# Performance work log

Measured on AMD Instinct MI355X. Metric: run time of the kernel, lower is better.

The kernel has to match this reference:

```python
import jax, jax.numpy as jnp
import numpy as np

HIDDEN = 1024
NUM_HEADS = 16
HEAD_DIM = HIDDEN // NUM_HEADS
EPS = 1e-05


def setup_inputs() -> dict:
    key = jax.random.key(0)
    ks = jax.random.split(key, 6)
    B, S = 4, 2048
    x = jax.random.normal(ks[0], (B, S, HIDDEN), dtype=jnp.float32)
    # trunc_normal_(std=0.02) approximated by scaled normal
    w_in = jax.random.normal(ks[1], (3 * HIDDEN, HIDDEN), dtype=jnp.float32) * 0.02
    b_in = jax.random.normal(ks[2], (3 * HIDDEN,), dtype=jnp.float32) * 0.02
    w_norm = jnp.ones((HIDDEN,), dtype=jnp.float32)
    lim = 1.0 / np.sqrt(HIDDEN)
    w_out = jax.random.uniform(ks[3], (HIDDEN, HIDDEN), dtype=jnp.float32, minval=-lim, maxval=lim)
    b_out = jax.random.uniform(ks[4], (HIDDEN,), dtype=jnp.float32, minval=-lim, maxval=lim)
    return {"x": x, "w_in": w_in, "b_in": b_in, "w_norm": w_norm, "w_out": w_out, "b_out": b_out}


def _rms_norm(x, w, eps):
    var = jnp.mean(jnp.square(x), axis=-1, keepdims=True)
    return x * jax.lax.rsqrt(var + eps) * w


def reference(x, w_in, b_in, w_norm, w_out, b_out):
    B, S, _ = x.shape
    xn = _rms_norm(x, w_norm, EPS)
    qkv = jnp.einsum('bsd,ed->bse', xn, w_in) + b_in  # [B,S,3*HIDDEN]
    q, k, v = jnp.split(qkv, 3, axis=-1)
    # [B,S,H*D] -> [B,H,S,D]
    def split_heads(t):
        return t.reshape(B, S, NUM_HEADS, HEAD_DIM).transpose(0, 2, 1, 3)
    q, k, v = split_heads(q), split_heads(k), split_heads(v)
    scale = 1.0 / np.sqrt(HEAD_DIM)
    scores = jnp.einsum('bhqd,bhkd->bhqk', q, k) * scale
    attn = jax.nn.softmax(scores, axis=-1)
    o = jnp.einsum('bhqk,bhkd->bhqd', attn, v)
    o = o.transpose(0, 2, 1, 3).reshape(B, S, HIDDEN)
    return jnp.einsum('bsd,ed->bse', o, w_out) + b_out
```

## Files before the change

### kernel.cpp

```cpp
#include <hip/hip_runtime.h>
#include <stdint.h>

typedef short bf16x4 __attribute__((ext_vector_type(4)));
typedef short bf16x8 __attribute__((ext_vector_type(8)));
typedef _Float16 f16x8 __attribute__((ext_vector_type(8)));
typedef float f32x4 __attribute__((ext_vector_type(4)));
typedef float f32x16 __attribute__((ext_vector_type(16)));
typedef unsigned int u32x4 __attribute__((ext_vector_type(4)));
typedef unsigned int u32x2 __attribute__((ext_vector_type(2)));

#if __has_builtin(__builtin_amdgcn_exp2f)
#define EXP2 __builtin_amdgcn_exp2f
#else
#define EXP2 exp2f
#endif

__device__ __forceinline__ short f2bf(float f) {
  union { float f; uint32_t u; } v; v.f = f;
  uint32_t r = (v.u + 0x7fffu + ((v.u >> 16) & 1u)) >> 16;
  return (short)(uint16_t)r;
}

__device__ __forceinline__ unsigned cvtpk_bf16(float lo, float hi) {
  unsigned r;
  asm("v_cvt_pk_bf16_f32 %0, %1, %2" : "=v"(r) : "v"(lo), "v"(hi));
  return r;
}

#if __has_builtin(__builtin_amdgcn_permlane32_swap)
__device__ __forceinline__ void plane32_swap(unsigned& a, unsigned& b) {
  u32x2 r = __builtin_amdgcn_permlane32_swap(a, b, false, false);
  a = r[0]; b = r[1];
}
__device__ __forceinline__ float xhalf_max(float x) {
  unsigned xu = __builtin_bit_cast(unsigned, x);
  u32x2 r = __builtin_amdgcn_permlane32_swap(xu, xu, false, false);
  return fmaxf(__builtin_bit_cast(float, r[0]), __builtin_bit_cast(float, r[1]));
}
__device__ __forceinline__ float xhalf_sum(float x) {
  unsigned xu = __builtin_bit_cast(unsigned, x);
  u32x2 r = __builtin_amdgcn_permlane32_swap(xu, xu, false, false);
  return __builtin_bit_cast(float, r[0]) + __builtin_bit_cast(float, r[1]);
}
#else
__device__ __forceinline__ void plane32_swap(unsigned& a, unsigned& b) {
  asm("s_nop 1\n\tv_permlane32_swap_b32 %0, %1" : "+v"(a), "+v"(b));
}
__device__ __forceinline__ float xhalf_max(float x) { return fmaxf(x, __shfl_xor(x, 32, 64)); }
__device__ __forceinline__ float xhalf_sum(float x) { return x + __shfl_xor(x, 32, 64); }
#endif

__device__ __forceinline__ float fmax3(float a, float b, float c) {
  return fmaxf(fmaxf(a, b), c);
}

__device__ __forceinline__ f32x16 zero16() {
  f32x16 z;
#pragma unroll
  for (int i = 0; i < 16; ++i) z[i] = 0.f;
  return z;
}

__device__ __forceinline__ void gld_lds16(const void* g, void* l) {
  __builtin_amdgcn_global_load_lds(
      (__attribute__((address_space(1))) const void*)g,
      (__attribute__((address_space(3))) void*)l, 16, 0, 0);
}

__global__ __launch_bounds__(256) void k_rmsnorm(const float* __restrict__ x,
                                                 const float* __restrict__ wn,
                                                 short* __restrict__ xn) {
  const int row = blockIdx.x;
  const int t = threadIdx.x;
  const float4 v = reinterpret_cast<const float4*>(x + (size_t)row * 1024)[t];
  float ss = v.x * v.x + v.y * v.y + v.z * v.z + v.w * v.w;
#pragma unroll
  for (int m = 32; m >= 1; m >>= 1) ss += __shfl_xor(ss, m, 64);
  __shared__ float red[4];
  if ((t & 63) == 0) red[t >> 6] = ss;
  __syncthreads();
  const float tot = red[0] + red[1] + red[2] + red[3];
  const float rr = rsqrtf(tot * (1.0f / 1024.0f) + 1e-5f);
  const float4 g = reinterpret_cast<const float4*>(wn)[t];
  bf16x4 o;
  o[0] = f2bf(v.x * rr * g.x);
  o[1] = f2bf(v.y * rr * g.y);
  o[2] = f2bf(v.z * rr * g.z);
  o[3] = f2bf(v.w * rr * g.w);
  reinterpret_cast<bf16x4*>(xn + (size_t)row * 1024)[t] = o;
}

__global__ __launch_bounds__(256) void k_cast_bf(const float* __restrict__ in,
                                                 short* __restrict__ out, int n4) {
  int i = blockIdx.x * 256 + threadIdx.x;
  if (i >= n4) return;
  float4 v = reinterpret_cast<const float4*>(in)[i];
  bf16x4 o;
  o[0] = f2bf(v.x); o[1] = f2bf(v.y); o[2] = f2bf(v.z); o[3] = f2bf(v.w);
  reinterpret_cast<bf16x4*>(out)[i] = o;
}

__global__ __launch_bounds__(256) void k_cast_f16(const float* __restrict__ in,
                                                  _Float16* __restrict__ out, int n4) {
  int i = blockIdx.x * 256 + threadIdx.x;
  if (i >= n4) return;
  float4 v = reinterpret_cast<const float4*>(in)[i];
  _Float16 o[4] = {(_Float16)v.x, (_Float16)v.y, (_Float16)v.z, (_Float16)v.w};
  reinterpret_cast<ulong1*>(out)[i] = *reinterpret_cast<ulong1*>(o);
}

__global__ __launch_bounds__(256) void k_gemm_qkv(const short* __restrict__ A,
                                                  const short* __restrict__ B,
                                                  const float* __restrict__ bias,
                                                  short* __restrict__ qb,
                                                  short* __restrict__ kb,
                                                  short* __restrict__ vb) {
  __shared__ __align__(16) short As[128 * 32];
  __shared__ __align__(16) short Bs[128 * 32];
  const int t = threadIdx.x;
  const int orig = blockIdx.y * 24 + blockIdx.x;
  const int swz = (orig & 7) * 192 + (orig >> 3);
  const long bn0 = (long)(swz % 24) * 128;
  const long bm0 = (long)(swz / 24) * 128;
  const int w = t >> 6, l = t & 63;
  const int wr = (w >> 1) * 64, wc = (w & 1) * 64;
  const int lm = l & 15, h = l >> 4;
  f32x4 acc[4][4];
#pragma unroll
  for (int i = 0; i < 4; ++i)
#pragma unroll
    for (int j = 0; j < 4; ++j) acc[i][j] = (f32x4){0.f, 0.f, 0.f, 0.f};
  const int srow = t >> 2, scol = (t & 3) * 8;
  const short* Ag = A + (bm0 + srow) * 1024 + scol;
  const short* Bg = B + (bn0 + srow) * 1024 + scol;
  short* AsP = As + t * 8;
  short* BsP = Bs + t * 8;
  for (int kt = 0; kt < 32; ++kt) {
    const int k0 = kt << 5;
    gld_lds16(Ag + k0, AsP);
    gld_lds16(Ag + k0 + 64 * 1024, AsP + 2048);
    gld_lds16(Bg + k0, BsP);
    gld_lds16(Bg + k0 + 64 * 1024, BsP + 2048);
    __syncthreads();
    bf16x8 af[4], bfr[4];
#pragma unroll
    for (int mi = 0; mi < 4; ++mi)
      af[mi] = *reinterpret_cast<const bf16x8*>(As + (wr + mi * 16 + lm) * 32 + h * 8);
#pragma unroll
    for (int ni = 0; ni < 4; ++ni)
      bfr[ni] = *reinterpret_cast<const bf16x8*>(Bs + (wc + ni * 16 + lm) * 32 + h * 8);
    __builtin_amdgcn_s_setprio(1);
#pragma unroll
    for (int mi = 0; mi < 4; ++mi)
#pragma unroll
      for (int ni = 0; ni < 4; ++ni)
        acc[mi][ni] = __builtin_amdgcn_mfma_f32_16x16x32_bf16(af[mi], bfr[ni], acc[mi][ni], 0, 0, 0);
    __builtin_amdgcn_s_setprio(0);
    __syncthreads();
  }
#pragma unroll
  for (int ni = 0; ni < 4; ++ni) {
    const int ncol = (int)bn0 + wc + ni * 16 + lm;
    const float bv = bias[ncol];
    const int which = ncol >> 10;
    const int e = ncol & 1023;
#pragma unroll
    for (int mi = 0; mi < 4; ++mi) {
#pragma unroll
      for (int r = 0; r < 4; ++r) {
        const long mrow = bm0 + wr + mi * 16 + h * 4 + r;
        const float val = acc[mi][ni][r] + bv;
        const long off = (((mrow >> 11) * 16 + (e >> 6)) * 2048 + (mrow & 2047)) * 64 + (e & 63);
        if (which == 0) qb[off] = f2bf(val * 0.18033688011112042f);
        else if (which == 1) kb[off] = f2bf(val);
        else vb[off] = f2bf(val);
      }
    }
  }
}

__global__ __launch_bounds__(256) void k_gemm_out(const _Float16* __restrict__ A,
                                                  const _Float16* __restrict__ B,
                                                  const float* __restrict__ bias,
                                                  float* __restrict__ outp) {
  __shared__ __align__(16) _Float16 As[128 * 32];
  __shared__ __align__(16) _Float16 Bs[128 * 32];
  const int t = threadIdx.x;
  const int orig = blockIdx.y * 8 + blockIdx.x;
  const int swz = (orig & 7) * 64 + (orig >> 3);
  const long bn0 = (long)(swz % 8) * 128;
  const long bm0 = (long)(swz / 8) * 128;
  const int w = t >> 6, l = t & 63;
  const int wr = (w >> 1) * 64, wc = (w & 1) * 64;
  const int lm = l & 15, h = l >> 4;
  f32x4 acc[4][4];
#pragma unroll
  for (int i = 0; i < 4; ++i)
#pragma unroll
    for (int j = 0; j < 4; ++j) acc[i][j] = (f32x4){0.f, 0.f, 0.f, 0.f};
  const int srow = t >> 2, scol = (t & 3) * 8;
  const _Float16* Ag = A + (bm0 + srow) * 1024 + scol;
  const _Float16* Bg = B + (bn0 + srow) * 1024 + scol;
  _Float16* AsP = As + t * 8;
  _Float16* BsP = Bs + t * 8;
  for (int kt = 0; kt < 32; ++kt) {
    const int k0 = kt << 5;
    gld_lds16(Ag + k0, AsP);
    gld_lds16(Ag + k0 + 64 * 1024, AsP + 2048);
    gld_lds16(Bg + k0, BsP);
    gld_lds16(Bg + k0 + 64 * 1024, BsP + 2048);
    __syncthreads();
    f16x8 af[4], bfr[4];
#pragma unroll
    for (int mi = 0; mi < 4; ++mi)
      af[mi] = *reinterpret_cast<const f16x8*>(As + (wr + mi * 16 + lm) * 32 + h * 8);
#pragma unroll
    for (int ni = 0; ni < 4; ++ni)
      bfr[ni] = *reinterpret_cast<const f16x8*>(Bs + (wc + ni * 16 + lm) * 32 + h * 8);
    __builtin_amdgcn_s_setprio(1);
#pragma unroll
    for (int mi = 0; mi < 4; ++mi)
#pragma unroll
      for (int ni = 0; ni < 4; ++ni)
        acc[mi][ni] = __builtin_amdgcn_mfma_f32_16x16x32_f16(af[mi], bfr[ni], acc[mi][ni], 0, 0, 0);
    __builtin_amdgcn_s_setprio(0);
    __syncthreads();
  }
#pragma unroll
  for (int ni = 0; ni < 4; ++ni) {
    const int ncol = (int)bn0 + wc + ni * 16 + lm;
    const float bv = bias[ncol];
#pragma unroll
    for (int mi = 0; mi < 4; ++mi) {
#pragma unroll
      for (int r = 0; r < 4; ++r) {
        const long mrow = bm0 + wr + mi * 16 + h * 4 + r;
        outp[mrow * 1024 + ncol] = acc[mi][ni][r] + bv;
      }
    }
  }
}

__global__ __launch_bounds__(256) void k_transpose_v(const short* __restrict__ v,
                                                     short* __restrict__ vt) {
  __shared__ short tile[64][72];
  const int bh = blockIdx.y, st = blockIdx.x;
  const int t = threadIdx.x;
  const int r = t >> 2, c0 = (t & 3) * 16;
  const short* src = v + ((size_t)(bh * 2048 + st * 64 + r)) * 64 + c0;
  bf16x8 a = *reinterpret_cast<const bf16x8*>(src);
  bf16x8 b = *reinterpret_cast<const bf16x8*>(src + 8);
#pragma unroll
  for (int j = 0; j < 8; ++j) tile[r][c0 + j] = a[j];
#pragma unroll
  for (int j = 0; j < 8; ++j) tile[r][c0 + 8 + j] = b[j];
  __syncthreads();
  __align__(16) short tmp[16];
#pragma unroll
  for (int j = 0; j < 16; ++j) tmp[j] = tile[c0 + j][r];
  short* dst = vt + ((size_t)(bh * 64 + r)) * 2048 + st * 64 + c0;
  *reinterpret_cast<bf16x8*>(dst) = *reinterpret_cast<const bf16x8*>(tmp);
  *reinterpret_cast<bf16x8*>(dst + 8) = *reinterpret_cast<const bf16x8*>(tmp + 8);
}

__global__ __launch_bounds__(256) void k_attn(const short* __restrict__ q,
                                              const short* __restrict__ k,
                                              const short* __restrict__ vt,
                                              _Float16* __restrict__ o) {
  __shared__ __align__(16) short Ks[2][4096];
  __shared__ __align__(16) short Vs[2][4096];
  const int bh = blockIdx.y;
  const int qt = blockIdx.x;
  const int t = threadIdx.x;
  const int w = t >> 6, l = t & 63;
  const int lq = l & 31, hh = l >> 5;
  const int xr = lq & 7;
  const int qrow = qt * 128 + w * 32 + lq;

  const short* qp = q + ((size_t)(bh * 2048 + qrow)) * 64 + hh * 8;
  bf16x8 qf[4];
#pragma unroll
  for (int db = 0; db < 4; ++db) qf[db] = *reinterpret_cast<const bf16x8*>(qp + db * 16);

  const int gg0 = w * 128 + l, gg1 = gg0 + 64;
  const int u0 = gg0 ^ ((gg0 >> 3) & 7);
  const int u1 = gg1 ^ ((gg1 >> 3) & 7);
  const short* kh = k + (size_t)bh * 2048 * 64;
  const short* vh = vt + (size_t)bh * 64 * 2048;
  const short* ksrc0 = kh + u0 * 8;
  const short* ksrc1 = kh + u1 * 8;
  const short* vsrc0 = vh + (gg0 >> 3) * 2048 + (u0 & 7) * 8;
  const short* vsrc1 = vh + (gg1 >> 3) * 2048 + (u1 & 7) * 8;

  int koff[2][4], voff[2][4];
#pragma unroll
  for (int ks = 0; ks < 2; ++ks)
#pragma unroll
    for (int db = 0; db < 4; ++db)
      koff[ks][db] = ((ks * 32 + lq) * 8 + ((db * 2 + hh) ^ xr)) * 8;
#pragma unroll
  for (int dt = 0; dt < 2; ++dt)
#pragma unroll
    for (int kg = 0; kg < 4; ++kg)
      voff[dt][kg] = ((dt * 32 + lq) * 8 + ((kg * 2 + hh) ^ xr)) * 8;

  f32x16 oa0 = zero16(), oa1 = zero16();
  float mr = -1e30f, lr = 0.f;

  gld_lds16(ksrc0, &Ks[0][gg0 * 8]);
  gld_lds16(ksrc1, &Ks[0][gg1 * 8]);
  gld_lds16(vsrc0, &Vs[0][gg0 * 8]);
  gld_lds16(vsrc1, &Vs[0][gg1 * 8]);
  __syncthreads();

  int cur = 0;
  for (int kt = 0; kt < 32; ++kt) {
    const int kn = (kt + 1) & 31;
    const int nb = cur ^ 1;
    gld_lds16(ksrc0 + kn * 4096, &Ks[nb][gg0 * 8]);
    gld_lds16(ksrc1 + kn * 4096, &Ks[nb][gg1 * 8]);
    gld_lds16(vsrc0 + kn * 64, &Vs[nb][gg0 * 8]);
    gld_lds16(vsrc1 + kn * 64, &Vs[nb][gg1 * 8]);

    const short* kb_ = Ks[cur];
    const short* vb_ = Vs[cur];
    f32x16 s0 = zero16(), s1 = zero16();
    __builtin_amdgcn_s_setprio(1);
#pragma unroll
    for (int db = 0; db < 4; ++db) {
      bf16x8 kf = *reinterpret_cast<const bf16x8*>(kb_ + koff[0][db]);
      s0 = __builtin_amdgcn_mfma_f32_32x32x16_bf16(kf, qf[db], s0, 0, 0, 0);
    }
#pragma unroll
    for (int db = 0; db < 4; ++db) {
      bf16x8 kf = *reinterpret_cast<const bf16x8*>(kb_ + koff[1][db]);
      s1 = __builtin_amdgcn_mfma_f32_32x32x16_bf16(kf, qf[db], s1, 0, 0, 0);
    }
    __builtin_amdgcn_s_setprio(0);
    float m8[8];
#pragma unroll
    for (int i = 0; i < 8; ++i)
      m8[i] = fmax3(fmaxf(s0[i], s0[i + 8]), s1[i], s1[i + 8]);
    float t0 = fmax3(m8[0], m8[1], m8[2]);
    float t1 = fmax3(m8[3], m8[4], m8[5]);
    float tm = fmax3(fmax3(m8[6], m8[7], t0), t1, -1e30f);
    tm = xhalf_max(tm);
    if (!__all(tm <= mr + 8.f)) {
      const float mn = fmaxf(mr, tm);
      const float corr = EXP2(mr - mn);
      lr *= corr;
#pragma unroll
      for (int r = 0; r < 16; ++r) { oa0[r] *= corr; oa1[r] *= corr; }
      mr = mn;
    }
#pragma unroll
    for (int r = 0; r < 16; ++r) {
      s0[r] = EXP2(s0[r] - mr);
      s1[r] = EXP2(s1[r] - mr);
    }
    float a8[8];
#pragma unroll
    for (int i = 0; i < 8; ++i)
      a8[i] = (s0[i] + s0[i + 8]) + (s1[i] + s1[i + 8]);
    lr += ((a8[0] + a8[4]) + (a8[1] + a8[5])) + ((a8[2] + a8[6]) + (a8[3] + a8[7]));
    __builtin_amdgcn_s_setprio(1);
#pragma unroll
    for (int kg = 0; kg < 4; ++kg) {
      const f32x16& sv = (kg & 2) ? s1 : s0;
      const int b0 = (kg & 1) * 8;
      unsigned w0 = cvtpk_bf16(sv[b0 + 0], sv[b0 + 1]);
      unsigned w1 = cvtpk_bf16(sv[b0 + 2], sv[b0 + 3]);
      unsigned w2 = cvtpk_bf16(sv[b0 + 4], sv[b0 + 5]);
      unsigned w3 = cvtpk_bf16(sv[b0 + 6], sv[b0 + 7]);
      plane32_swap(w0, w2);
      plane32_swap(w1, w3);
      u32x4 pw = {w0, w1, w2, w3};
      bf16x8 pf = *reinterpret_cast<bf16x8*>(&pw);
      bf16x8 vf0 = *reinterpret_cast<const bf16x8*>(vb_ + voff[0][kg]);
      oa0 = __builtin_amdgcn_mfma_f32_32x32x16_bf16(vf0, pf, oa0, 0, 0, 0);
      bf16x8 vf1 = *reinterpret_cast<const bf16x8*>(vb_ + voff[1][kg]);
      oa1 = __builtin_amdgcn_mfma_f32_32x32x16_bf16(vf1, pf, oa1, 0, 0, 0);
    }
    __builtin_amdgcn_s_setprio(0);
    __syncthreads();
    cur = nb;
  }
  const float lt = xhalf_sum(lr);
  const float inv = 1.0f / lt;
  const int b = bh >> 4, hd = bh & 15;
  _Float16* ob = o + ((size_t)(b * 2048 + qrow)) * 1024 + hd * 64;
#pragma unroll
  for (int r2 = 0; r2 < 16; ++r2) {
    const int d0 = (r2 & 3) + 8 * (r2 >> 2) + 4 * hh;
    ob[d0] = (_Float16)(oa0[r2] * inv);
    ob[d0 + 32] = (_Float16)(oa1[r2] * inv);
  }
}

extern "C" void kernel_launch(void* const* d_in, const int* in_sizes, int n_in,
                              void* d_out, int out_size, void* d_ws, size_t ws_size,
                              hipStream_t stream) {
  const float* x = (const float*)d_in[0];
  const float* w_in = (const float*)d_in[1];
  const float* b_in = (const float*)d_in[2];
  const float* w_norm = (const float*)d_in[3];
  const float* w_out = (const float*)d_in[4];
  const float* b_out = (const float*)d_in[5];
  float* out = (float*)d_out;
  char* ws = (char*)d_ws;
  short* xn = (short*)(ws);
  short* win_b = (short*)(ws + 16777216);
  _Float16* wout_h = (_Float16*)(ws + 23068672);
  short* qb = (short*)(ws + 25165824);
  short* kb = (short*)(ws + 41943040);
  short* vb = (short*)(ws + 58720256);
  short* vt = (short*)(ws + 75497472);
  _Float16* ob = (_Float16*)vb;

  k_cast_bf<<<3072, 256, 0, stream>>>(w_in, win_b, 786432);
  k_cast_f16<<<1024, 256, 0, stream>>>(w_out, wout_h, 262144);
  k_rmsnorm<<<8192, 256, 0, stream>>>(x, w_norm, xn);
  k_gemm_qkv<<<dim3(24, 64), 256, 0, stream>>>(xn, win_b, b_in, qb, kb, vb);
  k_transpose_v<<<dim3(32, 64), 256, 0, stream>>>(vb, vt);
  k_attn<<<dim3(16, 64), 256, 0, stream>>>(qb, kb, vt, ob);
  k_gemm_out<<<dim3(8, 64), 256, 0, stream>>>(ob, wout_h, b_out, out);
}
```

Before: 241.9 us.

## Double per-wave query rows in attention, halve KV tile size

Each wave now handles 64 query rows (two 32-row MFMA groups) against a 32-key tile, so every K and V fragment read from LDS feeds two MFMAs instead of one. The block covers 256 queries, which halves the grid and the total K/V global-to-LDS traffic. The LDS tile shrinks to 32 keys per stage and the loop runs 64 iterations with a new swizzle for V, and launch bounds request 2 blocks per CU. The cost is twice the accumulator registers, more barriers per key, and fewer blocks (512) to spread across the CUs.

```diff
diff --git a/kernel.cpp b/kernel.cpp
--- a/kernel.cpp
+++ b/kernel.cpp
@@ -52,6 +52,24 @@
 
 __device__ __forceinline__ float fmax3(float a, float b, float c) {
   return fmaxf(fmaxf(a, b), c);
+}
+
+__device__ __forceinline__ float tmax16(const f32x16& s) {
+  float a0 = fmax3(s[0], s[1], s[2]);
+  float a1 = fmax3(s[3], s[4], s[5]);
+  float a2 = fmax3(s[6], s[7], s[8]);
+  float a3 = fmax3(s[9], s[10], s[11]);
+  float a4 = fmax3(s[12], s[13], s[14]);
+  float b0 = fmax3(a0, a1, s[15]);
+  float b1 = fmax3(a2, a3, a4);
+  return fmaxf(b0, b1);
+}
+__device__ __forceinline__ float tsum16(const f32x16& s) {
+  float a0 = (s[0] + s[1]) + (s[2] + s[3]);
+  float a1 = (s[4] + s[5]) + (s[6] + s[7]);
+  float a2 = (s[8] + s[9]) + (s[10] + s[11]);
+  float a3 = (s[12] + s[13]) + (s[14] + s[15]);
+  return (a0 + a1) + (a2 + a3);
 }
 
 __device__ __forceinline__ f32x16 zero16() {
@@ -263,64 +281,62 @@
   *reinterpret_cast<bf16x8*>(dst + 8) = *reinterpret_cast<const bf16x8*>(tmp + 8);
 }
 
-__global__ __launch_bounds__(256) void k_attn(const short* __restrict__ q,
-                                              const short* __restrict__ k,
-                                              const short* __restrict__ vt,
-                                              _Float16* __restrict__ o) {
-  __shared__ __align__(16) short Ks[2][4096];
-  __shared__ __align__(16) short Vs[2][4096];
+__global__ __launch_bounds__(256, 2) void k_attn(const short* __restrict__ q,
+                                                 const short* __restrict__ k,
+                                                 const short* __restrict__ vt,
+                                                 _Float16* __restrict__ o) {
+  __shared__ __align__(16) short Ks[2][2048];
+  __shared__ __align__(16) short Vs[2][2048];
   const int bh = blockIdx.y;
   const int qt = blockIdx.x;
   const int t = threadIdx.x;
   const int w = t >> 6, l = t & 63;
   const int lq = l & 31, hh = l >> 5;
   const int xr = lq & 7;
-  const int qrow = qt * 128 + w * 32 + lq;
-
-  const short* qp = q + ((size_t)(bh * 2048 + qrow)) * 64 + hh * 8;
-  bf16x8 qf[4];
-#pragma unroll
-  for (int db = 0; db < 4; ++db) qf[db] = *reinterpret_cast<const bf16x8*>(qp + db * 16);
-
-  const int gg0 = w * 128 + l, gg1 = gg0 + 64;
-  const int u0 = gg0 ^ ((gg0 >> 3) & 7);
-  const int u1 = gg1 ^ ((gg1 >> 3) & 7);
+  const int qbase = qt * 256 + w * 64;
+
+  bf16x8 qf[2][4];
+#pragma unroll
+  for (int qh = 0; qh < 2; ++qh) {
+    const short* qp = q + ((size_t)(bh * 2048 + qbase + qh * 32 + lq)) * 64 + hh * 8;
+#pragma unroll
+    for (int db = 0; db < 4; ++db)
+      qf[qh][db] = *reinterpret_cast<const bf16x8*>(qp + db * 16);
+  }
+
+  const int gg = t;
+  const int uK = gg ^ ((gg >> 3) & 7);
+  const int vrow = gg >> 2;
+  const int vcol = (gg & 3) ^ (vrow & 3);
   const short* kh = k + (size_t)bh * 2048 * 64;
   const short* vh = vt + (size_t)bh * 64 * 2048;
-  const short* ksrc0 = kh + u0 * 8;
-  const short* ksrc1 = kh + u1 * 8;
-  const short* vsrc0 = vh + (gg0 >> 3) * 2048 + (u0 & 7) * 8;
-  const short* vsrc1 = vh + (gg1 >> 3) * 2048 + (u1 & 7) * 8;
-
-  int koff[2][4], voff[2][4];
-#pragma unroll
-  for (int ks = 0; ks < 2; ++ks)
-#pragma unroll
-    for (int db = 0; db < 4; ++db)
-      koff[ks][db] = ((ks * 32 + lq) * 8 + ((db * 2 + hh) ^ xr)) * 8;
+  const short* ksrc = kh + uK * 8;
+  const short* vsrc = vh + vrow * 2048 + vcol * 8;
+
+  int koff[4], voff[2][2];
+#pragma unroll
+  for (int db = 0; db < 4; ++db)
+    koff[db] = (lq * 8 + ((db * 2 + hh) ^ xr)) * 8;
 #pragma unroll
   for (int dt = 0; dt < 2; ++dt)
 #pragma unroll
-    for (int kg = 0; kg < 4; ++kg)
-      voff[dt][kg] = ((dt * 32 + lq) * 8 + ((kg * 2 + hh) ^ xr)) * 8;
-
-  f32x16 oa0 = zero16(), oa1 = zero16();
-  float mr = -1e30f, lr = 0.f;
-
-  gld_lds16(ksrc0, &Ks[0][gg0 * 8]);
-  gld_lds16(ksrc1, &Ks[0][gg1 * 8]);
-  gld_lds16(vsrc0, &Vs[0][gg0 * 8]);
-  gld_lds16(vsrc1, &Vs[0][gg1 * 8]);
+    for (int kg = 0; kg < 2; ++kg)
+      voff[dt][kg] = ((dt * 32 + lq) * 4 + ((kg * 2 + hh) ^ (lq & 3))) * 8;
+
+  f32x16 oa00 = zero16(), oa01 = zero16();
+  f32x16 oa10 = zero16(), oa11 = zero16();
+  float mr0 = -1e30f, mr1 = -1e30f, lr0 = 0.f, lr1 = 0.f;
+
+  gld_lds16(ksrc, &Ks[0][gg * 8]);
+  gld_lds16(vsrc, &Vs[0][gg * 8]);
   __syncthreads();
 
   int cur = 0;
-  for (int kt = 0; kt < 32; ++kt) {
-    const int kn = (kt + 1) & 31;
+  for (int kt = 0; kt < 64; ++kt) {
+    const int kn = (kt + 1) & 63;
     const int nb = cur ^ 1;
-    gld_lds16(ksrc0 + kn * 4096, &Ks[nb][gg0 * 8]);
-    gld_lds16(ksrc1 + kn * 4096, &Ks[nb][gg1 * 8]);
-    gld_lds16(vsrc0 + kn * 64, &Vs[nb][gg0 * 8]);
-    gld_lds16(vsrc1 + kn * 64, &Vs[nb][gg1 * 8]);
+    gld_lds16(ksrc + kn * 2048, &Ks[nb][gg * 8]);
+    gld_lds16(vsrc + kn * 32, &Vs[nb][gg * 8]);
 
     const short* kb_ = Ks[cur];
     const short* vb_ = Vs[cur];
@@ -328,72 +344,74 @@
     __builtin_amdgcn_s_setprio(1);
 #pragma unroll
     for (int db = 0; db < 4; ++db) {
-      bf16x8 kf = *reinterpret_cast<const bf16x8*>(kb_ + koff[0][db]);
-      s0 = __builtin_amdgcn_mfma_f32_32x32x16_bf16(kf, qf[db], s0, 0, 0, 0);
-    }
-#pragma unroll
-    for (int db = 0; db < 4; ++db) {
-      bf16x8 kf = *reinterpret_cast<const bf16x8*>(kb_ + koff[1][db]);
-      s1 = __builtin_amdgcn_mfma_f32_32x32x16_bf16(kf, qf[db], s1, 0, 0, 0);
+      bf16x8 kf = *reinterpret_cast<const bf16x8*>(kb_ + koff[db]);
+      s0 = __builtin_amdgcn_mfma_f32_32x32x16_bf16(kf, qf[0][db], s0, 0, 0, 0);
+      s1 = __builtin_amdgcn_mfma_f32_32x32x16_bf16(kf, qf[1][db], s1, 0, 0, 0);
     }
     __builtin_amdgcn_s_setprio(0);
-    float m8[8];
-#pragma unroll
-    for (int i = 0; i < 8; ++i)
-      m8[i] = fmax3(fmaxf(s0[i], s0[i + 8]), s1[i], s1[i + 8]);
-    float t0 = fmax3(m8[0], m8[1], m8[2]);
-    float t1 = fmax3(m8[3], m8[4], m8[5]);
-    float tm = fmax3(fmax3(m8[6], m8[7], t0), t1, -1e30f);
-    tm = xhalf_max(tm);
-    if (!__all(tm <= mr + 8.f)) {
-      const float mn = fmaxf(mr, tm);
-      const float corr = EXP2(mr - mn);
-      lr *= corr;
-#pragma unroll
-      for (int r = 0; r < 16; ++r) { oa0[r] *= corr; oa1[r] *= corr; }
-      mr = mn;
+    float tm0 = xhalf_max(tmax16(s0));
+    float tm1 = xhalf_max(tmax16(s1));
+    if (!__all((tm0 <= mr0 + 8.f) && (tm1 <= mr1 + 8.f))) {
+      const float mn0 = fmaxf(mr0, tm0), mn1 = fmaxf(mr1, tm1);
+      const float c0 = EXP2(mr0 - mn0), c1 = EXP2(mr1 - mn1);
+      lr0 *= c0; lr1 *= c1;
+#pragma unroll
+      for (int r = 0; r < 16; ++r) {
+        oa00[r] *= c0; oa01[r] *= c0;
+        oa10[r] *= c1; oa11[r] *= c1;
+      }
+      mr0 = mn0; mr1 = mn1;
     }
 #pragma unroll
     for (int r = 0; r < 16; ++r) {
-      s0[r] = EXP2(s0[r] - mr);
-      s1[r] = EXP2(s1[r] - mr);
-    }
-    float a8[8];
-#pragma unroll
-    for (int i = 0; i < 8; ++i)
-      a8[i] = (s0[i] + s0[i + 8]) + (s1[i] + s1[i + 8]);
-    lr += ((a8[0] + a8[4]) + (a8[1] + a8[5])) + ((a8[2] + a8[6]) + (a8[3] + a8[7]));
+      s0[r] = EXP2(s0[r] - mr0);
+      s1[r] = EXP2(s1[r] - mr1);
+    }
+    lr0 += tsum16(s0);
+    lr1 += tsum16(s1);
     __builtin_amdgcn_s_setprio(1);
 #pragma unroll
-    for (int kg = 0; kg < 4; ++kg) {
-      const f32x16& sv = (kg & 2) ? s1 : s0;
-      const int b0 = (kg & 1) * 8;
-      unsigned w0 = cvtpk_bf16(sv[b0 + 0], sv[b0 + 1]);
-      unsigned w1 = cvtpk_bf16(sv[b0 + 2], sv[b0 + 3]);
-      unsigned w2 = cvtpk_bf16(sv[b0 + 4], sv[b0 + 5]);
-      unsigned w3 = cvtpk_bf16(sv[b0 + 6], sv[b0 + 7]);
-      plane32_swap(w0, w2);
-      plane32_swap(w1, w3);
-      u32x4 pw = {w0, w1, w2, w3};
-      bf16x8 pf = *reinterpret_cast<bf16x8*>(&pw);
+    for (int kg = 0; kg < 2; ++kg) {
+      const int b0 = kg * 8;
+      unsigned p00 = cvtpk_bf16(s0[b0 + 0], s0[b0 + 1]);
+      unsigned p01 = cvtpk_bf16(s0[b0 + 2], s0[b0 + 3]);
+      unsigned p02 = cvtpk_bf16(s0[b0 + 4], s0[b0 + 5]);
+      unsigned p03 = cvtpk_bf16(s0[b0 + 6], s0[b0 + 7]);
+      plane32_swap(p00, p02);
+      plane32_swap(p01, p03);
+      u32x4 pw0 = {p00, p01, p02, p03};
+      bf16x8 pf0 = *reinterpret_cast<bf16x8*>(&pw0);
+      unsigned p10 = cvtpk_bf16(s1[b0 + 0], s1[b0 + 1]);
+      unsigned p11 = cvtpk_bf16(s1[b0 + 2], s1[b0 + 3]);
+      unsigned p12 = cvtpk_bf16(s1[b0 + 4], s1[b0 + 5]);
+      unsigned p13 = cvtpk_bf16(s1[b0 + 6], s1[b0 + 7]);
+      plane32_swap(p10, p12);
+      plane32_swap(p11, p13);
+      u32x4 pw1 = {p10, p11, p12, p13};
+      bf16x8 pf1 = *reinterpret_cast<bf16x8*>(&pw1);
       bf16x8 vf0 = *reinterpret_cast<const bf16x8*>(vb_ + voff[0][kg]);
-      oa0 = __builtin_amdgcn_mfma_f32_32x32x16_bf16(vf0, pf, oa0, 0, 0, 0);
+      oa00 = __builtin_amdgcn_mfma_f32_32x32x16_bf16(vf0, pf0, oa00, 0, 0, 0);
+      oa10 = __builtin_amdgcn_mfma_f32_32x32x16_bf16(vf0, pf1, oa10, 0, 0, 0);
       bf16x8 vf1 = *reinterpret_cast<const bf16x8*>(vb_ + voff[1][kg]);
-      oa1 = __builtin_amdgcn_mfma_f32_32x32x16_bf16(vf1, pf, oa1, 0, 0, 0);
+      oa01 = __builtin_amdgcn_mfma_f32_32x32x16_bf16(vf1, pf0, oa01, 0, 0, 0);
+      oa11 = __builtin_amdgcn_mfma_f32_32x32x16_bf16(vf1, pf1, oa11, 0, 0, 0);
     }
     __builtin_amdgcn_s_setprio(0);
     __syncthreads();
     cur = nb;
   }
-  const float lt = xhalf_sum(lr);
-  const float inv = 1.0f / lt;
+  const float inv0 = 1.0f / xhalf_sum(lr0);
+  const float inv1 = 1.0f / xhalf_sum(lr1);
   const int b = bh >> 4, hd = bh & 15;
-  _Float16* ob = o + ((size_t)(b * 2048 + qrow)) * 1024 + hd * 64;
+  _Float16* ob0 = o + ((size_t)(b * 2048 + qbase + lq)) * 1024 + hd * 64;
+  _Float16* ob1 = ob0 + 32 * 1024;
 #pragma unroll
   for (int r2 = 0; r2 < 16; ++r2) {
     const int d0 = (r2 & 3) + 8 * (r2 >> 2) + 4 * hh;
-    ob[d0] = (_Float16)(oa0[r2] * inv);
-    ob[d0 + 32] = (_Float16)(oa1[r2] * inv);
+    ob0[d0] = (_Float16)(oa00[r2] * inv0);
+    ob0[d0 + 32] = (_Float16)(oa01[r2] * inv0);
+    ob1[d0] = (_Float16)(oa10[r2] * inv1);
+    ob1[d0 + 32] = (_Float16)(oa11[r2] * inv1);
   }
 }
 
@@ -422,6 +440,6 @@
   k_rmsnorm<<<8192, 256, 0, stream>>>(x, w_norm, xn);
   k_gemm_qkv<<<dim3(24, 64), 256, 0, stream>>>(xn, win_b, b_in, qb, kb, vb);
   k_transpose_v<<<dim3(32, 64), 256, 0, stream>>>(vb, vt);
-  k_attn<<<dim3(16, 64), 256, 0, stream>>>(qb, kb, vt, ob);
+  k_attn<<<dim3(8, 64), 256, 0, stream>>>(qb, kb, vt, ob);
   k_gemm_out<<<dim3(8, 64), 256, 0, stream>>>(ob, wout_h, b_out, out);
 }
```

Result: faster. 231.5 us (-4.3%).
